# Kernel tuning notes

Hardware: AMD Instinct MI355X
Metric: run time of the kernel (lower is better)

The kernel has to match this reference:

```python
import jax, jax.numpy as jnp
import numpy as np

B, CIN, H, W = 8, 128, 64, 64
COUT, KH, KW = 128, 3, 3
STRIDE = (1, 1)
PAD = (1, 1)
DIL = (1, 1)
GROUPS = 1
OFFSET_GROUPS = 1

def _out_size(i, k, s, p, d):
    return (i + 2 * p - d * (k - 1) - 1) // s + 1

HO = _out_size(H, KH, STRIDE[0], PAD[0], DIL[0])
WO = _out_size(W, KW, STRIDE[1], PAD[1], DIL[1])


def setup_inputs() -> dict:
    key = jax.random.key(0)
    k1, k2, k3, k4 = jax.random.split(key, 4)
    x = jax.random.normal(k1, (B, CIN, H, W), jnp.float32)
    offset = jax.random.normal(k2, (B, 2 * OFFSET_GROUPS * KH * KW, HO, WO), jnp.float32)
    fan_in = (CIN // GROUPS) * KH * KW
    bound = 1.0 / np.sqrt(fan_in)
    weight = jax.random.uniform(k3, (COUT, CIN // GROUPS, KH, KW), jnp.float32, -bound, bound)
    bias = jax.random.uniform(k4, (COUT,), jnp.float32, -bound, bound)
    return {"x": x, "offset": offset, "weight": weight, "bias": bias}


def _deform_conv2d(x, offset, weight, bias):
    Bn, Cin, Hi, Wi = x.shape
    K = KH * KW
    Goff, Gw = OFFSET_GROUPS, GROUPS
    Cpg = Cin // Goff

    # base sampling positions (before learned offsets)
    ys = jnp.arange(HO, dtype=jnp.float32) * STRIDE[0] - PAD[0]  # [HO]
    xs = jnp.arange(WO, dtype=jnp.float32) * STRIDE[1] - PAD[1]  # [WO]
    base_y = jnp.repeat(jnp.arange(KH, dtype=jnp.float32) * DIL[0], KW)  # [K]
    base_x = jnp.tile(jnp.arange(KW, dtype=jnp.float32) * DIL[1], KH)    # [K]

    # offsets: channel layout is 2*(g*K + k) + {0: dy, 1: dx}
    off = offset.reshape(Bn, Goff, K, 2, HO, WO)
    py = base_y[None, None, :, None, None] + ys[None, None, None, :, None] + off[:, :, :, 0]  # [B,Goff,K,HO,WO]
    px = base_x[None, None, :, None, None] + xs[None, None, None, None, :] + off[:, :, :, 1]

    y0 = jnp.floor(py)
    x0 = jnp.floor(px)
    ly = py - y0  # fractional weights
    lx = px - x0

    xg = x.reshape(Bn, Goff, Cpg, Hi * Wi)

    def gather_one(img, lin):  # img [Cpg, H*W], lin [K,HO,WO] -> [Cpg,K,HO,WO]
        return img[:, lin]

    gather = jax.vmap(jax.vmap(gather_one))  # over B and Goff

    def corner(yi, xi, w):
        # zero-padding semantics: out-of-bounds corner contributes 0
        mask = (yi >= 0) & (yi < Hi) & (xi >= 0) & (xi < Wi)
        iy = jnp.clip(yi, 0, Hi - 1).astype(jnp.int32)
        ix = jnp.clip(xi, 0, Wi - 1).astype(jnp.int32)
        lin = iy * Wi + ix  # [B,Goff,K,HO,WO]
        wm = (w * mask.astype(x.dtype))[:, :, None]  # broadcast over channel axis
        return gather(xg, lin) * wm  # [B,Goff,Cpg,K,HO,WO]

    val = (corner(y0, x0, (1 - ly) * (1 - lx))
           + corner(y0, x0 + 1, (1 - ly) * lx)
           + corner(y0 + 1, x0, ly * (1 - lx))
           + corner(y0 + 1, x0 + 1, ly * lx))  # [B,Goff,Cpg,K,HO,WO]

    # grouped conv accumulate
    val = val.reshape(Bn, Gw, Cin // Gw, K, HO, WO)
    wg = weight.reshape(Gw, COUT // Gw, Cin // Gw, K)
    out = jnp.einsum('bgckhw,gock->bgohw', val, wg).reshape(Bn, COUT, HO, WO)
    return out + bias[None, :, None, None]


def reference(x, offset, weight, bias):
    return _deform_conv2d(x, offset, weight, bias)
```

## Files before the change

kernel.cpp:

```cpp
#include <hip/hip_runtime.h>

typedef unsigned int   u32;
typedef unsigned short u16;
typedef short bf16x8 __attribute__((ext_vector_type(8)));
typedef float f32x4  __attribute__((ext_vector_type(4)));
typedef float f32x2  __attribute__((ext_vector_type(2)));

#define CIN   128
#define COUT  128
#define Hh    64
#define Ww    64
#define Bb    8
#define NKPOS 9
#define XT_ELEMS (Bb*Hh*Ww*CIN)

__device__ __forceinline__ float bflo(u32 u){ return __uint_as_float(u << 16); }
__device__ __forceinline__ float bfhi(u32 u){ return __uint_as_float(u & 0xffff0000u); }

__device__ __forceinline__ u32 pack2(float a, float b){
    u32 lo = __float_as_uint(a) + 0x8000u;
    u32 hi = __float_as_uint(b) + 0x8000u;
    return __builtin_amdgcn_perm(hi, lo, 0x07060302u);
}
__device__ __forceinline__ u16 tobf(float a){
    u32 ua = __float_as_uint(a);
    ua += 0x7fffu + ((ua >> 16) & 1u);
    return (u16)(ua >> 16);
}

__global__ __launch_bounds__(256) void k_transpose(const float* __restrict__ x,
                                                   u16* __restrict__ xT){
    __shared__ float lds[64*132];
    int bi = blockIdx.x;
    int hb = bi & 63, b = bi >> 6;
    int tid = threadIdx.x;

    {
        int r = tid >> 1, cq = tid & 1;
        const float* xp = x + ((size_t)(b*128 + r))*4096 + hb*64 + cq*32;
        float4 v[8];
#pragma unroll
        for (int k = 0; k < 8; ++k) v[k] = *(const float4*)(xp + k*4);
        float* dst = lds + (cq*32)*132 + r;
#pragma unroll
        for (int k = 0; k < 8; ++k){
            dst[(k*4+0)*132] = v[k].x;
            dst[(k*4+1)*132] = v[k].y;
            dst[(k*4+2)*132] = v[k].z;
            dst[(k*4+3)*132] = v[k].w;
        }
    }
    __syncthreads();
    {
        int s = tid >> 2, kq = tid & 3;
        const float* src = lds + s*132 + kq*32;
        u32 r16[16];
#pragma unroll
        for (int k = 0; k < 8; ++k){
            float4 v = *(const float4*)(src + k*4);
            r16[k*2  ] = pack2(v.x, v.y);
            r16[k*2+1] = pack2(v.z, v.w);
        }
        u32* dst = (u32*)xT + ((size_t)(b*4096 + hb*64 + s))*64 + kq*16;
#pragma unroll
        for (int k = 0; k < 4; ++k)
            *(uint4*)(dst + k*4) = *(uint4*)&r16[k*4];
    }
}

__global__ __launch_bounds__(256) void k_wprep(const float* __restrict__ w,
                                               u16* __restrict__ Wt){
    int gid = blockIdx.x*256 + threadIdx.x;
    int jf   = gid & 7;
    int lane = (gid >> 3) & 63;
    int mt   = (gid >> 9) & 7;
    int kt   = gid >> 12;
    int m  = mt*16 + (lane & 15);
    int kk = (lane >> 4)*8 + jf;
    int ck = kt*32 + kk;
    int kpos = ck >> 7;
    int cin  = ck & 127;
    Wt[gid] = tobf(w[((size_t)m*128 + cin)*9 + kpos]);
}

__global__ __launch_bounds__(256, 2)
void k_main(const float* __restrict__ off, const float* __restrict__ bias,
            const u16* __restrict__ xT, const u16* __restrict__ Wt,
            float* __restrict__ out){
    __shared__ u32 Vsm[2][4*64*20];

    int tid = threadIdx.x, bi = blockIdx.x;
    int b = bi & 7, t = bi >> 3;
    int s0 = t * 64;

    int p = tid >> 2, qt = tid & 3;
    const u16* xb = xT + (size_t)b * (Hh*Ww*CIN);
    const float* offp = off + ((size_t)b*18)*4096 + s0 + p;

    int lane = tid & 63, wave = tid >> 6;
    int wm = wave >> 1, wn = wave & 1;
    int quad = lane >> 4, l16 = lane & 15;

    f32x4 acc[4][2];
#pragma unroll
    for (int i = 0; i < 4; ++i)
#pragma unroll
        for (int j = 0; j < 2; ++j) acc[i][j] = {0.f,0.f,0.f,0.f};

    int   aaS[2][4];
    float wtS[2][4];
    float dyN, dxN;
    uint4 ring[4][4];
    uint4 av[2][4];

    auto load_off = [&](int kpos){
        const float* op = offp + (size_t)(2*kpos)*4096;
        dyN = op[0];
        dxN = op[4096];
    };
    auto state = [&](int kpos, int st){
        float dy = dyN, dx = dxN;
        int kh = kpos / 3, kw = kpos - kh*3;
        float py = (float)(t + kh - 1) + dy;
        float px = (float)(p + kw - 1) + dx;
        float y0f = floorf(py), x0f = floorf(px);
        float ly = py - y0f, lx = px - x0f;
        int y0 = (int)y0f, x0 = (int)x0f;
        int y1 = y0 + 1,  x1 = x0 + 1;
        float my0 = (y0 >= 0 && y0 < Hh) ? 1.f : 0.f;
        float my1 = (y1 >= 0 && y1 < Hh) ? 1.f : 0.f;
        float mx0 = (x0 >= 0 && x0 < Ww) ? 1.f : 0.f;
        float mx1 = (x1 >= 0 && x1 < Ww) ? 1.f : 0.f;
        float oy = 1.f - ly, ox = 1.f - lx;
        wtS[st][0] = oy*ox*my0*mx0;
        wtS[st][1] = oy*lx*my0*mx1;
        wtS[st][2] = ly*ox*my1*mx0;
        wtS[st][3] = ly*lx*my1*mx1;
        int cy0 = min(max(y0,0),Hh-1), cy1 = min(max(y1,0),Hh-1);
        int cx0 = min(max(x0,0),Ww-1), cx1 = min(max(x1,0),Ww-1);
        aaS[st][0] = (cy0*Ww + cx0)*CIN;
        aaS[st][1] = (cy0*Ww + cx1)*CIN;
        aaS[st][2] = (cy1*Ww + cx0)*CIN;
        aaS[st][3] = (cy1*Ww + cx1)*CIN;
    };
    auto gather = [&](int st){
#pragma unroll
        for (int c = 0; c < 4; ++c){
            const u16* xc = xb + aaS[st][c] + qt*32;
#pragma unroll
            for (int s = 0; s < 4; ++s)
                ring[c][s] = *(const uint4*)(xc + s*8);
        }
    };
    auto loadA = [&](int gc, uint4 a[4]){
        const u16* wp = Wt + (size_t)((gc*8 + wm*4)*64 + lane)*8;
#pragma unroll
        for (int i = 0; i < 4; ++i)
            a[i] = *(const uint4*)(wp + (size_t)i*64*8);
    };
    auto blend_store = [&](int st, int buf){
        u32* dst = &Vsm[buf][qt*1280 + p*20];
#pragma unroll
        for (int s = 0; s < 4; ++s){
            u32 r4[4];
#pragma unroll
            for (int d = 0; d < 4; ++d){
                f32x2 s2 = {0.f, 0.f};
#pragma unroll
                for (int c = 0; c < 4; ++c){
                    u32 u = ((const u32*)&ring[c][s])[d];
                    f32x2 v  = { bflo(u), bfhi(u) };
                    f32x2 w2 = { wtS[st][c], wtS[st][c] };
                    s2 += w2 * v;
                }
                r4[d] = pack2(s2.x, s2.y);
            }
            *(uint2*)(dst + s*4    ) = *(uint2*)&r4[0];
            *(uint2*)(dst + s*4 + 2) = *(uint2*)&r4[2];
        }
    };

    load_off(0);
    state(0, 0);
    gather(0);
    load_off(1);
    state(1, 1);
    blend_store(0, 0);
    loadA(0, av[0]);

#pragma unroll
    for (int g = 0; g < NKPOS; ++g){
        __syncthreads();
        if (g + 1 < NKPOS) gather((g + 1) & 1);
        if (g + 2 < NKPOS) load_off(g + 2);

#pragma unroll
        for (int c = 0; c < 4; ++c){
            int gc = g*4 + c;
            if (gc + 1 < 4*NKPOS) loadA(gc + 1, av[(gc + 1) & 1]);

            uint4 braw[2];
#pragma unroll
            for (int j = 0; j < 2; ++j)
                braw[j] = *(const uint4*)&Vsm[g & 1][c*1280 + ((wn*2 + j)*16 + l16)*20 + quad*4];
#pragma unroll
            for (int i = 0; i < 4; ++i){
                bf16x8 avv = __builtin_bit_cast(bf16x8, av[gc & 1][i]);
#pragma unroll
                for (int j = 0; j < 2; ++j){
                    bf16x8 bv = __builtin_bit_cast(bf16x8, braw[j]);
                    acc[i][j] = __builtin_amdgcn_mfma_f32_16x16x32_bf16(avv, bv, acc[i][j], 0, 0, 0);
                }
            }
        }

        if (g + 2 < NKPOS) state(g + 2, g & 1);
        if (g + 1 < NKPOS) blend_store((g + 1) & 1, (g + 1) & 1);
    }

#pragma unroll
    for (int i = 0; i < 4; ++i){
        int cout0 = (wm*4 + i)*16 + quad*4;
#pragma unroll
        for (int j = 0; j < 2; ++j){
            int pcol = (wn*2 + j)*16 + l16;
            size_t obase = ((size_t)(b*COUT + cout0))*4096 + (s0 + pcol);
#pragma unroll
            for (int r = 0; r < 4; ++r)
                out[obase + (size_t)r*4096] = acc[i][j][r] + bias[cout0 + r];
        }
    }
}

extern "C" void kernel_launch(void* const* d_in, const int* in_sizes, int n_in,
                              void* d_out, int out_size, void* d_ws, size_t ws_size,
                              hipStream_t stream){
    const float* x    = (const float*)d_in[0];
    const float* off  = (const float*)d_in[1];
    const float* w    = (const float*)d_in[2];
    const float* bias = (const float*)d_in[3];
    float* out = (float*)d_out;

    u16* xT = (u16*)d_ws;
    u16* Wt = xT + XT_ELEMS;

    k_transpose<<<dim3(512), dim3(256), 0, stream>>>(x, xT);
    k_wprep    <<<dim3(576), dim3(256), 0, stream>>>(w, Wt);
    k_main     <<<dim3(512), dim3(256), 0, stream>>>(off, bias, xT, Wt, out);
}
```

Baseline: 113.0 us.

## Split fused deformable sampling and GEMM into separate sample and GEMM kernels

Replaces the fused kernel, which sampled bilinear values into shared memory and ran MFMA in the same loop, with two kernels. A highly parallel sampling kernel writes the full bf16 im2col-style tensor V (about 75 MB) to global memory, and a separate GEMM kernel streams V and the weights through a double-buffered LDS tile. The intent is to decouple latency-bound gathers from the matrix work and raise occupancy for the gathers. The cost is a large extra global write and read of V plus an additional launch.

```diff
diff --git a/kernel.cpp b/kernel.cpp
--- a/kernel.cpp
+++ b/kernel.cpp
@@ -12,7 +12,10 @@
 #define Ww    64
 #define Bb    8
 #define NKPOS 9
+#define NCHUNK 36
 #define XT_ELEMS (Bb*Hh*Ww*CIN)
+#define WT_ELEMS (NCHUNK*8*64*8)
+#define V_ELEMS ((size_t)Bb*8*9*4096*16)
 
 __device__ __forceinline__ float bflo(u32 u){ return __uint_as_float(u << 16); }
 __device__ __forceinline__ float bfhi(u32 u){ return __uint_as_float(u & 0xffff0000u); }
@@ -35,8 +38,7 @@
     int hb = bi & 63, b = bi >> 6;
     int tid = threadIdx.x;
 
-    {
-        int r = tid >> 1, cq = tid & 1;
+    {   int r = tid >> 1, cq = tid & 1;
         const float* xp = x + ((size_t)(b*128 + r))*4096 + hb*64 + cq*32;
         float4 v[8];
 #pragma unroll
@@ -51,8 +53,7 @@
         }
     }
     __syncthreads();
-    {
-        int s = tid >> 2, kq = tid & 3;
+    {   int s = tid >> 2, kq = tid & 3;
         const float* src = lds + s*132 + kq*32;
         u32 r16[16];
 #pragma unroll
@@ -83,139 +84,138 @@
     Wt[gid] = tobf(w[((size_t)m*128 + cin)*9 + kpos]);
 }
 
+__global__ __launch_bounds__(256, 6)
+void k_sample(const float* __restrict__ off, const u16* __restrict__ xT,
+              u16* __restrict__ V){
+    int tid = threadIdx.x, bi = blockIdx.x;
+    int b  = bi & 7;
+    int q  = bi >> 3;
+    int kpos = q % 9;
+    int pb   = q / 9;
+    int cg   = tid & 7;
+    int pos  = pb*32 + (tid >> 3);
+    int ho = pos >> 6, wo = pos & 63;
+
+    size_t ob = ((size_t)(b*18 + 2*kpos))*4096 + pos;
+    float dy = off[ob];
+    float dx = off[ob + 4096];
+
+    int kh = kpos / 3, kw = kpos - kh*3;
+    float py = (float)(ho + kh - 1) + dy;
+    float px = (float)(wo + kw - 1) + dx;
+    float y0f = floorf(py), x0f = floorf(px);
+    float ly = py - y0f, lx = px - x0f;
+    int y0 = (int)y0f, x0 = (int)x0f;
+    int y1 = y0 + 1,  x1 = x0 + 1;
+    float my0 = (y0 >= 0 && y0 < Hh) ? 1.f : 0.f;
+    float my1 = (y1 >= 0 && y1 < Hh) ? 1.f : 0.f;
+    float mx0 = (x0 >= 0 && x0 < Ww) ? 1.f : 0.f;
+    float mx1 = (x1 >= 0 && x1 < Ww) ? 1.f : 0.f;
+    float oy = 1.f - ly, ox = 1.f - lx;
+    float wt[4] = { oy*ox*my0*mx0, oy*lx*my0*mx1, ly*ox*my1*mx0, ly*lx*my1*mx1 };
+    int cy0 = min(max(y0,0),Hh-1), cy1 = min(max(y1,0),Hh-1);
+    int cx0 = min(max(x0,0),Ww-1), cx1 = min(max(x1,0),Ww-1);
+    int aa[4] = { (cy0*Ww + cx0)*CIN, (cy0*Ww + cx1)*CIN,
+                  (cy1*Ww + cx0)*CIN, (cy1*Ww + cx1)*CIN };
+
+    const u16* xb = xT + (size_t)b*(Hh*Ww*CIN) + cg*16;
+    uint4 g[4][2];
+#pragma unroll
+    for (int c = 0; c < 4; ++c){
+        const u16* xc = xb + aa[c];
+        g[c][0] = *(const uint4*)(xc);
+        g[c][1] = *(const uint4*)(xc + 8);
+    }
+
+    u32 res[8];
+#pragma unroll
+    for (int d = 0; d < 8; ++d){
+        f32x2 s2 = {0.f, 0.f};
+#pragma unroll
+        for (int c = 0; c < 4; ++c){
+            u32 u = ((const u32*)&g[c][0])[d];
+            f32x2 v  = { bflo(u), bfhi(u) };
+            f32x2 w2 = { wt[c], wt[c] };
+            s2 += w2 * v;
+        }
+        res[d] = pack2(s2.x, s2.y);
+    }
+
+    u16* vp = V + ((((size_t)(b*8 + cg)*9 + kpos)*4096) + pos)*16;
+    *(uint4*)(vp    ) = *(uint4*)&res[0];
+    *(uint4*)(vp + 8) = *(uint4*)&res[4];
+}
+
 __global__ __launch_bounds__(256, 2)
-void k_main(const float* __restrict__ off, const float* __restrict__ bias,
-            const u16* __restrict__ xT, const u16* __restrict__ Wt,
-            float* __restrict__ out){
-    __shared__ u32 Vsm[2][4*64*20];
+void k_gemm(const u16* __restrict__ V, const u16* __restrict__ Wt,
+            const float* __restrict__ bias, float* __restrict__ out){
+    __shared__ u32 Bsm[2][1280];
 
     int tid = threadIdx.x, bi = blockIdx.x;
-    int b = bi & 7, t = bi >> 3;
-    int s0 = t * 64;
-
-    int p = tid >> 2, qt = tid & 3;
-    const u16* xb = xT + (size_t)b * (Hh*Ww*CIN);
-    const float* offp = off + ((size_t)b*18)*4096 + s0 + p;
-
+    int b = bi & 7, pt = bi >> 3;
     int lane = tid & 63, wave = tid >> 6;
     int wm = wave >> 1, wn = wave & 1;
     int quad = lane >> 4, l16 = lane & 15;
 
+    int sS = tid >> 7, rowS = (tid >> 1) & 63, halfS = tid & 1;
+
     f32x4 acc[4][2];
 #pragma unroll
     for (int i = 0; i < 4; ++i)
 #pragma unroll
         for (int j = 0; j < 2; ++j) acc[i][j] = {0.f,0.f,0.f,0.f};
 
-    int   aaS[2][4];
-    float wtS[2][4];
-    float dyN, dxN;
-    uint4 ring[4][4];
-    uint4 av[2][4];
-
-    auto load_off = [&](int kpos){
-        const float* op = offp + (size_t)(2*kpos)*4096;
-        dyN = op[0];
-        dxN = op[4096];
+    auto loadB = [&](int kc, uint4& r){
+        int kpos = kc >> 2, cg0 = (kc & 3)*2;
+        const u16* vp = V + ((((size_t)(b*8 + cg0 + sS)*9 + kpos)*4096)
+                             + pt*64 + rowS)*16 + halfS*8;
+        r = *(const uint4*)vp;
     };
-    auto state = [&](int kpos, int st){
-        float dy = dyN, dx = dxN;
-        int kh = kpos / 3, kw = kpos - kh*3;
-        float py = (float)(t + kh - 1) + dy;
-        float px = (float)(p + kw - 1) + dx;
-        float y0f = floorf(py), x0f = floorf(px);
-        float ly = py - y0f, lx = px - x0f;
-        int y0 = (int)y0f, x0 = (int)x0f;
-        int y1 = y0 + 1,  x1 = x0 + 1;
-        float my0 = (y0 >= 0 && y0 < Hh) ? 1.f : 0.f;
-        float my1 = (y1 >= 0 && y1 < Hh) ? 1.f : 0.f;
-        float mx0 = (x0 >= 0 && x0 < Ww) ? 1.f : 0.f;
-        float mx1 = (x1 >= 0 && x1 < Ww) ? 1.f : 0.f;
-        float oy = 1.f - ly, ox = 1.f - lx;
-        wtS[st][0] = oy*ox*my0*mx0;
-        wtS[st][1] = oy*lx*my0*mx1;
-        wtS[st][2] = ly*ox*my1*mx0;
-        wtS[st][3] = ly*lx*my1*mx1;
-        int cy0 = min(max(y0,0),Hh-1), cy1 = min(max(y1,0),Hh-1);
-        int cx0 = min(max(x0,0),Ww-1), cx1 = min(max(x1,0),Ww-1);
-        aaS[st][0] = (cy0*Ww + cx0)*CIN;
-        aaS[st][1] = (cy0*Ww + cx1)*CIN;
-        aaS[st][2] = (cy1*Ww + cx0)*CIN;
-        aaS[st][3] = (cy1*Ww + cx1)*CIN;
+    auto storeB = [&](const uint4& r, int buf){
+        *(uint4*)&Bsm[buf][sS*640 + rowS*10 + halfS*4] = r;
     };
-    auto gather = [&](int st){
-#pragma unroll
-        for (int c = 0; c < 4; ++c){
-            const u16* xc = xb + aaS[st][c] + qt*32;
-#pragma unroll
-            for (int s = 0; s < 4; ++s)
-                ring[c][s] = *(const uint4*)(xc + s*8);
-        }
-    };
-    auto loadA = [&](int gc, uint4 a[4]){
-        const u16* wp = Wt + (size_t)((gc*8 + wm*4)*64 + lane)*8;
+    auto loadA = [&](int kc, uint4 a[4]){
+        const u16* wp = Wt + (size_t)((kc*8 + wm*4)*64 + lane)*8;
 #pragma unroll
         for (int i = 0; i < 4; ++i)
             a[i] = *(const uint4*)(wp + (size_t)i*64*8);
     };
-    auto blend_store = [&](int st, int buf){
-        u32* dst = &Vsm[buf][qt*1280 + p*20];
-#pragma unroll
-        for (int s = 0; s < 4; ++s){
-            u32 r4[4];
-#pragma unroll
-            for (int d = 0; d < 4; ++d){
-                f32x2 s2 = {0.f, 0.f};
-#pragma unroll
-                for (int c = 0; c < 4; ++c){
-                    u32 u = ((const u32*)&ring[c][s])[d];
-                    f32x2 v  = { bflo(u), bfhi(u) };
-                    f32x2 w2 = { wtS[st][c], wtS[st][c] };
-                    s2 += w2 * v;
-                }
-                r4[d] = pack2(s2.x, s2.y);
+
+    uint4 ringB[2], avC[4], avN[4];
+    loadB(0, ringB[0]);
+    loadA(0, avC);
+    storeB(ringB[0], 0);
+    loadB(1, ringB[1]);
+    loadA(1, avN);
+    __syncthreads();
+
+    for (int kc = 0; kc < NCHUNK; ++kc){
+        int c1 = kc + 1, c2 = kc + 2;
+        if (c2 < NCHUNK) loadB(c2, ringB[kc & 1]);
+
+        uint4 braw[2];
+#pragma unroll
+        for (int j = 0; j < 2; ++j){
+            int n = wn*32 + j*16 + l16;
+            braw[j] = *(const uint4*)&Bsm[kc & 1][(quad >> 1)*640 + n*10 + (quad & 1)*4];
+        }
+#pragma unroll
+        for (int i = 0; i < 4; ++i){
+            bf16x8 a = __builtin_bit_cast(bf16x8, avC[i]);
+#pragma unroll
+            for (int j = 0; j < 2; ++j){
+                bf16x8 bv = __builtin_bit_cast(bf16x8, braw[j]);
+                acc[i][j] = __builtin_amdgcn_mfma_f32_16x16x32_bf16(a, bv, acc[i][j], 0, 0, 0);
             }
-            *(uint2*)(dst + s*4    ) = *(uint2*)&r4[0];
-            *(uint2*)(dst + s*4 + 2) = *(uint2*)&r4[2];
-        }
-    };
-
-    load_off(0);
-    state(0, 0);
-    gather(0);
-    load_off(1);
-    state(1, 1);
-    blend_store(0, 0);
-    loadA(0, av[0]);
-
-#pragma unroll
-    for (int g = 0; g < NKPOS; ++g){
+        }
+
+        if (c1 < NCHUNK){
+            storeB(ringB[c1 & 1], c1 & 1);
+#pragma unroll
+            for (int i = 0; i < 4; ++i) avC[i] = avN[i];
+            if (c2 < NCHUNK) loadA(c2, avN);
+        }
         __syncthreads();
-        if (g + 1 < NKPOS) gather((g + 1) & 1);
-        if (g + 2 < NKPOS) load_off(g + 2);
-
-#pragma unroll
-        for (int c = 0; c < 4; ++c){
-            int gc = g*4 + c;
-            if (gc + 1 < 4*NKPOS) loadA(gc + 1, av[(gc + 1) & 1]);
-
-            uint4 braw[2];
-#pragma unroll
-            for (int j = 0; j < 2; ++j)
-                braw[j] = *(const uint4*)&Vsm[g & 1][c*1280 + ((wn*2 + j)*16 + l16)*20 + quad*4];
-#pragma unroll
-            for (int i = 0; i < 4; ++i){
-                bf16x8 avv = __builtin_bit_cast(bf16x8, av[gc & 1][i]);
-#pragma unroll
-                for (int j = 0; j < 2; ++j){
-                    bf16x8 bv = __builtin_bit_cast(bf16x8, braw[j]);
-                    acc[i][j] = __builtin_amdgcn_mfma_f32_16x16x32_bf16(avv, bv, acc[i][j], 0, 0, 0);
-                }
-            }
-        }
-
-        if (g + 2 < NKPOS) state(g + 2, g & 1);
-        if (g + 1 < NKPOS) blend_store((g + 1) & 1, (g + 1) & 1);
     }
 
 #pragma unroll
@@ -223,8 +223,8 @@
         int cout0 = (wm*4 + i)*16 + quad*4;
 #pragma unroll
         for (int j = 0; j < 2; ++j){
-            int pcol = (wn*2 + j)*16 + l16;
-            size_t obase = ((size_t)(b*COUT + cout0))*4096 + (s0 + pcol);
+            int pcol = wn*32 + j*16 + l16;
+            size_t obase = ((size_t)(b*COUT + cout0))*4096 + pt*64 + pcol;
 #pragma unroll
             for (int r = 0; r < 4; ++r)
                 out[obase + (size_t)r*4096] = acc[i][j][r] + bias[cout0 + r];
@@ -243,8 +243,10 @@
 
     u16* xT = (u16*)d_ws;
     u16* Wt = xT + XT_ELEMS;
-
-    k_transpose<<<dim3(512), dim3(256), 0, stream>>>(x, xT);
-    k_wprep    <<<dim3(576), dim3(256), 0, stream>>>(w, Wt);
-    k_main     <<<dim3(512), dim3(256), 0, stream>>>(off, bias, xT, Wt, out);
-}
+    u16* V  = Wt + WT_ELEMS;
+
+    k_transpose<<<dim3(512),  dim3(256), 0, stream>>>(x, xT);
+    k_wprep    <<<dim3(576),  dim3(256), 0, stream>>>(w, Wt);
+    k_sample   <<<dim3(9216), dim3(256), 0, stream>>>(off, xT, V);
+    k_gemm     <<<dim3(512),  dim3(256), 0, stream>>>(V, Wt, bias, out);
+}
```

After: 145.8 us. 1.29x slower.
